# Kernel optimization log

Measured on AMD Instinct MI355X. Metric: run time of the kernel, lower is better.

Reference implementation:

```python
import jax, jax.numpy as jnp
import numpy as np

B, S, E, WIN = 8, 2048, 512, 11  # batch, seq_len, emb_dim, window_size (odd)
PAD_VAL = 0.0  # padding_idx used as constant pad value in F.pad


def setup_inputs() -> dict:
    key = jax.random.key(0)
    k1, k2, k3 = jax.random.split(key, 3)
    x = jax.random.normal(k1, (B, S, E), dtype=jnp.float32)
    lim = 1.0 / np.sqrt(E * WIN)  # torch Linear default init bound
    # One independent Linear per timestep (deepcopy clones): stacked weights/bias
    W = jax.random.uniform(k2, (S, WIN, WIN * E), minval=-lim, maxval=lim, dtype=jnp.float32)
    b = jax.random.uniform(k3, (S, WIN), minval=-lim, maxval=lim, dtype=jnp.float32)
    return {"x": x, "W": W, "b": b}


def reference(x, W, b):
    ww = WIN // 2
    # pad sequence dim on both sides with padding_idx
    padded = jnp.pad(x, ((0, 0), (ww, ww), (0, 0)), constant_values=PAD_VAL)  # [B, S+2ww, E]
    # gather all sliding windows at once: windows[b,t,j,:] = padded[b, t+j, :]
    idx = jnp.arange(S)[:, None] + jnp.arange(WIN)[None, :]
    windows = padded[:, idx, :]
    flat = windows.reshape(B, S, WIN * E)                     # flattened window per position
    gates = jax.nn.sigmoid(jnp.einsum('bsf,swf->bsw', flat, W) + b)
    # gate * embeddings, sum over window, tanh
    score = jnp.einsum('bsw,bswe->bse', gates, windows)       # [B, S, E]
    return jnp.tanh(score)
```

## Files before the change

### kernel.cpp

```cpp
#include <hip/hip_runtime.h>
#include <math.h>

#define B_    8
#define S_    2048
#define E_    512
#define WIN_  11
#define WW    5
#define F4C   1408
#define E4C   128
#define NBLKA (S_ * WIN_)
#define CPX_A (NBLKA / 8)
#define PSTR  (B_ * WIN_)

template <int CTRL, int RMASK>
__device__ __forceinline__ float dpp_add(float v) {
    int sh = __builtin_amdgcn_update_dpp(0, __float_as_int(v),
                                         CTRL, RMASK, 0xF, true);
    return v + __int_as_float(sh);
}
__device__ __forceinline__ float wave_sum63(float v) {
    v = dpp_add<0x111, 0xF>(v);
    v = dpp_add<0x112, 0xF>(v);
    v = dpp_add<0x114, 0xF>(v);
    v = dpp_add<0x118, 0xF>(v);
    v = dpp_add<0x142, 0xA>(v);
    v = dpp_add<0x143, 0xC>(v);
    return v;
}

__global__ __launch_bounds__(256)
void win_gate_partial(const float* __restrict__ x,
                      const float* __restrict__ W,
                      float* __restrict__ P)
{
    const int bid = blockIdx.x;
    const int sw  = (bid & 7) * CPX_A + (bid >> 3);
    const int s   = sw / WIN_;
    const int wp  = sw - s * WIN_;

    const int tid  = threadIdx.x;
    const int wid  = tid >> 6;
    const int lane = tid & 63;

    float* __restrict__ Pblk = P + (size_t)sw * PSTR;

    const int row = s - WW + wp;
    if (row < 0 || row >= S_) {
        if (tid < PSTR) Pblk[tid] = 0.f;
        return;
    }

    const float4* __restrict__ X4 = reinterpret_cast<const float4*>(x);
    const float4* __restrict__ W4 = reinterpret_cast<const float4*>(W)
        + (size_t)s * (WIN_ * F4C) + (size_t)wp * E4C;

    __shared__ float4 Wlds[WIN_ * E4C];

    #pragma unroll
    for (int j = 0; j < 6; ++j) {
        const int m = j * 256 + tid;
        if (j < 5 || wid < 2) {
            const int w  = m >> 7;
            const int e4 = m & 127;
            const float4* src = W4 + (size_t)w * F4C + e4;
            __builtin_amdgcn_global_load_lds(
                (const __attribute__((address_space(1))) void*)src,
                (__attribute__((address_space(3))) void*)&Wlds[m],
                16, 0, 0);
        }
    }
    __syncthreads();

    const int w0   = wid * 3;
    const int wcnt = (wid == 3) ? 2 : 3;

    float4 wv[3][2];
    #pragma unroll
    for (int j = 0; j < 3; ++j)
        if (j < wcnt) {
            wv[j][0] = Wlds[(w0 + j) * E4C + lane];
            wv[j][1] = Wlds[(w0 + j) * E4C + lane + 64];
        }

    float acc[B_][3];
    #pragma unroll
    for (int b = 0; b < B_; ++b)
        #pragma unroll
        for (int j = 0; j < 3; ++j) acc[b][j] = 0.f;

    #pragma unroll
    for (int half = 0; half < 2; ++half) {
        float4 xv[4][2];
        #pragma unroll
        for (int bb = 0; bb < 4; ++bb) {
            const int b = half * 4 + bb;
            xv[bb][0] = X4[((size_t)b * S_ + row) * E4C + lane];
            xv[bb][1] = X4[((size_t)b * S_ + row) * E4C + lane + 64];
        }
        #pragma unroll
        for (int bb = 0; bb < 4; ++bb) {
            const int b = half * 4 + bb;
            #pragma unroll
            for (int j = 0; j < 3; ++j) {
                if (j < wcnt) {
                    float a = acc[b][j];
                    a = fmaf(xv[bb][0].x, wv[j][0].x, a);
                    a = fmaf(xv[bb][0].y, wv[j][0].y, a);
                    a = fmaf(xv[bb][0].z, wv[j][0].z, a);
                    a = fmaf(xv[bb][0].w, wv[j][0].w, a);
                    a = fmaf(xv[bb][1].x, wv[j][1].x, a);
                    a = fmaf(xv[bb][1].y, wv[j][1].y, a);
                    a = fmaf(xv[bb][1].z, wv[j][1].z, a);
                    a = fmaf(xv[bb][1].w, wv[j][1].w, a);
                    acc[b][j] = a;
                }
            }
        }
    }

    #pragma unroll
    for (int b = 0; b < B_; ++b)
        #pragma unroll
        for (int j = 0; j < 3; ++j)
            if (j < wcnt) acc[b][j] = wave_sum63(acc[b][j]);

    if (lane == 63) {
        #pragma unroll
        for (int b = 0; b < B_; ++b)
            #pragma unroll
            for (int j = 0; j < 3; ++j)
                if (j < wcnt) Pblk[b * WIN_ + w0 + j] = acc[b][j];
    }
}

__device__ __forceinline__ float tanh_fast(float v) {
    const float e = __expf(v + v);
    return 1.f - 2.f / (e + 1.f);
}

__global__ __launch_bounds__(256)
void win_score(const float* __restrict__ x,
               const float* __restrict__ bias,
               const float* __restrict__ P,
               float* __restrict__ out)
{
    const int bid = blockIdx.x;
    const int s   = (bid & 7) * (S_ / 8) + (bid >> 3);
    const int tid = threadIdx.x;

    __shared__ float Pl[WIN_ * PSTR];
    __shared__ float gates[PSTR];

    const float4* Ps = reinterpret_cast<const float4*>(P + (size_t)s * (WIN_ * PSTR));
    if (tid < (WIN_ * PSTR) / 4)
        reinterpret_cast<float4*>(Pl)[tid] = Ps[tid];
    __syncthreads();

    if (tid < PSTR) {
        const int w = tid % WIN_;
        float v = bias[s * WIN_ + w];
        #pragma unroll
        for (int wp = 0; wp < WIN_; ++wp) v += Pl[wp * PSTR + tid];
        gates[tid] = 1.f / (1.f + __expf(-v));
    }
    __syncthreads();

    const float4* __restrict__ X4   = reinterpret_cast<const float4*>(x);
    float4* __restrict__       OUT4 = reinterpret_cast<float4*>(out);

    #pragma unroll
    for (int it = 0; it < 4; ++it) {
        const int i  = tid + (it << 8);
        const int b  = i >> 7;
        const int e4 = i & 127;
        float4 sc = make_float4(0.f, 0.f, 0.f, 0.f);
        #pragma unroll
        for (int w = 0; w < WIN_; ++w) {
            const int r = s - WW + w;
            if (r >= 0 && r < S_) {
                const float g   = gates[b * WIN_ + w];
                const float4 xv = X4[((size_t)b * S_ + r) * E4C + e4];
                sc.x = fmaf(g, xv.x, sc.x);
                sc.y = fmaf(g, xv.y, sc.y);
                sc.z = fmaf(g, xv.z, sc.z);
                sc.w = fmaf(g, xv.w, sc.w);
            }
        }
        float4 o;
        o.x = tanh_fast(sc.x);
        o.y = tanh_fast(sc.y);
        o.z = tanh_fast(sc.z);
        o.w = tanh_fast(sc.w);
        OUT4[((size_t)b * S_ + s) * E4C + e4] = o;
    }
}

extern "C" void kernel_launch(void* const* d_in, const int* in_sizes, int n_in,
                              void* d_out, int out_size, void* d_ws, size_t ws_size,
                              hipStream_t stream)
{
    const float* x    = (const float*)d_in[0];
    const float* W    = (const float*)d_in[1];
    const float* bias = (const float*)d_in[2];
    float* out        = (float*)d_out;
    float* P          = (float*)d_ws;

    win_gate_partial<<<dim3(NBLKA), dim3(256), 0, stream>>>(x, W, P);
    win_score<<<dim3(S_), dim3(256), 0, stream>>>(x, bias, P, out);
}
```

Measured before the change: 158.5 us.

## Fuse gate partial and score kernels into one per-timestep kernel

Merges the two kernels into a single kernel with one block per timestep. That block loops over the 11 window positions, stages the weight slice in LDS each iteration and accumulates the gate logits in registers. This removes the partial-sum workspace round trip and one kernel launch. In exchange, grid parallelism drops from S*WIN blocks to S blocks, and each iteration serializes a weight load, a barrier and the compute with no double buffering, so latency hiding may suffer.

New measurement: 156.0 us. About the same (-1.6%).

```diff
diff --git a/kernel.cpp b/kernel.cpp
--- a/kernel.cpp
+++ b/kernel.cpp
@@ -8,8 +8,6 @@
 #define WW    5
 #define F4C   1408
 #define E4C   128
-#define NBLKA (S_ * WIN_)
-#define CPX_A (NBLKA / 8)
 #define PSTR  (B_ * WIN_)
 
 template <int CTRL, int RMASK>
@@ -28,59 +26,32 @@
     return v;
 }
 
+__device__ __forceinline__ float tanh_fast(float v) {
+    const float e = __expf(v + v);
+    return 1.f - 2.f / (e + 1.f);
+}
+
 __global__ __launch_bounds__(256)
-void win_gate_partial(const float* __restrict__ x,
-                      const float* __restrict__ W,
-                      float* __restrict__ P)
+void win_attn_fused(const float* __restrict__ x,
+                    const float* __restrict__ W,
+                    const float* __restrict__ bias,
+                    float* __restrict__ out)
 {
-    const int bid = blockIdx.x;
-    const int sw  = (bid & 7) * CPX_A + (bid >> 3);
-    const int s   = sw / WIN_;
-    const int wp  = sw - s * WIN_;
-
+    const int bid  = blockIdx.x;
+    const int s    = (bid & 7) * (S_ / 8) + (bid >> 3);
     const int tid  = threadIdx.x;
     const int wid  = tid >> 6;
     const int lane = tid & 63;
 
-    float* __restrict__ Pblk = P + (size_t)sw * PSTR;
+    const float4* __restrict__ X4 = reinterpret_cast<const float4*>(x);
+    const float4* __restrict__ Ws = reinterpret_cast<const float4*>(W)
+                                    + (size_t)s * (WIN_ * F4C);
 
-    const int row = s - WW + wp;
-    if (row < 0 || row >= S_) {
-        if (tid < PSTR) Pblk[tid] = 0.f;
-        return;
-    }
-
-    const float4* __restrict__ X4 = reinterpret_cast<const float4*>(x);
-    const float4* __restrict__ W4 = reinterpret_cast<const float4*>(W)
-        + (size_t)s * (WIN_ * F4C) + (size_t)wp * E4C;
-
-    __shared__ float4 Wlds[WIN_ * E4C];
-
-    #pragma unroll
-    for (int j = 0; j < 6; ++j) {
-        const int m = j * 256 + tid;
-        if (j < 5 || wid < 2) {
-            const int w  = m >> 7;
-            const int e4 = m & 127;
-            const float4* src = W4 + (size_t)w * F4C + e4;
-            __builtin_amdgcn_global_load_lds(
-                (const __attribute__((address_space(1))) void*)src,
-                (__attribute__((address_space(3))) void*)&Wlds[m],
-                16, 0, 0);
-        }
-    }
-    __syncthreads();
+    __shared__ float4 Wbuf[WIN_ * E4C];
+    __shared__ float gates[PSTR];
 
     const int w0   = wid * 3;
     const int wcnt = (wid == 3) ? 2 : 3;
-
-    float4 wv[3][2];
-    #pragma unroll
-    for (int j = 0; j < 3; ++j)
-        if (j < wcnt) {
-            wv[j][0] = Wlds[(w0 + j) * E4C + lane];
-            wv[j][1] = Wlds[(w0 + j) * E4C + lane + 64];
-        }
 
     float acc[B_][3];
     #pragma unroll
@@ -88,34 +59,64 @@
         #pragma unroll
         for (int j = 0; j < 3; ++j) acc[b][j] = 0.f;
 
-    #pragma unroll
-    for (int half = 0; half < 2; ++half) {
-        float4 xv[4][2];
+    #pragma unroll 1
+    for (int wp = 0; wp < WIN_; ++wp) {
         #pragma unroll
-        for (int bb = 0; bb < 4; ++bb) {
-            const int b = half * 4 + bb;
-            xv[bb][0] = X4[((size_t)b * S_ + row) * E4C + lane];
-            xv[bb][1] = X4[((size_t)b * S_ + row) * E4C + lane + 64];
+        for (int j = 0; j < 6; ++j) {
+            const int m = j * 256 + tid;
+            if (j < 5 || wid < 2) {
+                const int w  = m >> 7;
+                const int e4 = m & 127;
+                const float4* src = Ws + (size_t)w * F4C + wp * E4C + e4;
+                __builtin_amdgcn_global_load_lds(
+                    (const __attribute__((address_space(1))) void*)src,
+                    (__attribute__((address_space(3))) void*)&Wbuf[m],
+                    16, 0, 0);
+            }
         }
-        #pragma unroll
-        for (int bb = 0; bb < 4; ++bb) {
-            const int b = half * 4 + bb;
+        __syncthreads();
+
+        const int row = s - WW + wp;
+        if (row >= 0 && row < S_) {
+            float4 wv[3][2];
             #pragma unroll
-            for (int j = 0; j < 3; ++j) {
+            for (int j = 0; j < 3; ++j)
                 if (j < wcnt) {
-                    float a = acc[b][j];
-                    a = fmaf(xv[bb][0].x, wv[j][0].x, a);
-                    a = fmaf(xv[bb][0].y, wv[j][0].y, a);
-                    a = fmaf(xv[bb][0].z, wv[j][0].z, a);
-                    a = fmaf(xv[bb][0].w, wv[j][0].w, a);
-                    a = fmaf(xv[bb][1].x, wv[j][1].x, a);
-                    a = fmaf(xv[bb][1].y, wv[j][1].y, a);
-                    a = fmaf(xv[bb][1].z, wv[j][1].z, a);
-                    a = fmaf(xv[bb][1].w, wv[j][1].w, a);
-                    acc[b][j] = a;
+                    wv[j][0] = Wbuf[(w0 + j) * E4C + lane];
+                    wv[j][1] = Wbuf[(w0 + j) * E4C + lane + 64];
+                }
+
+            #pragma unroll
+            for (int half = 0; half < 2; ++half) {
+                float4 xv[4][2];
+                #pragma unroll
+                for (int bb = 0; bb < 4; ++bb) {
+                    const int b = half * 4 + bb;
+                    xv[bb][0] = X4[((size_t)b * S_ + row) * E4C + lane];
+                    xv[bb][1] = X4[((size_t)b * S_ + row) * E4C + lane + 64];
+                }
+                #pragma unroll
+                for (int bb = 0; bb < 4; ++bb) {
+                    const int b = half * 4 + bb;
+                    #pragma unroll
+                    for (int j = 0; j < 3; ++j) {
+                        if (j < wcnt) {
+                            float a = acc[b][j];
+                            a = fmaf(xv[bb][0].x, wv[j][0].x, a);
+                            a = fmaf(xv[bb][0].y, wv[j][0].y, a);
+                            a = fmaf(xv[bb][0].z, wv[j][0].z, a);
+                            a = fmaf(xv[bb][0].w, wv[j][0].w, a);
+                            a = fmaf(xv[bb][1].x, wv[j][1].x, a);
+                            a = fmaf(xv[bb][1].y, wv[j][1].y, a);
+                            a = fmaf(xv[bb][1].z, wv[j][1].z, a);
+                            a = fmaf(xv[bb][1].w, wv[j][1].w, a);
+                            acc[b][j] = a;
+                        }
+                    }
                 }
             }
         }
+        __syncthreads();
     }
 
     #pragma unroll
@@ -129,45 +130,18 @@
         for (int b = 0; b < B_; ++b)
             #pragma unroll
             for (int j = 0; j < 3; ++j)
-                if (j < wcnt) Pblk[b * WIN_ + w0 + j] = acc[b][j];
+                if (j < wcnt) gates[b * WIN_ + w0 + j] = acc[b][j];
     }
-}
-
-__device__ __forceinline__ float tanh_fast(float v) {
-    const float e = __expf(v + v);
-    return 1.f - 2.f / (e + 1.f);
-}
-
-__global__ __launch_bounds__(256)
-void win_score(const float* __restrict__ x,
-               const float* __restrict__ bias,
-               const float* __restrict__ P,
-               float* __restrict__ out)
-{
-    const int bid = blockIdx.x;
-    const int s   = (bid & 7) * (S_ / 8) + (bid >> 3);
-    const int tid = threadIdx.x;
-
-    __shared__ float Pl[WIN_ * PSTR];
-    __shared__ float gates[PSTR];
-
-    const float4* Ps = reinterpret_cast<const float4*>(P + (size_t)s * (WIN_ * PSTR));
-    if (tid < (WIN_ * PSTR) / 4)
-        reinterpret_cast<float4*>(Pl)[tid] = Ps[tid];
     __syncthreads();
 
     if (tid < PSTR) {
         const int w = tid % WIN_;
-        float v = bias[s * WIN_ + w];
-        #pragma unroll
-        for (int wp = 0; wp < WIN_; ++wp) v += Pl[wp * PSTR + tid];
+        const float v = gates[tid] + bias[s * WIN_ + w];
         gates[tid] = 1.f / (1.f + __expf(-v));
     }
     __syncthreads();
 
-    const float4* __restrict__ X4   = reinterpret_cast<const float4*>(x);
-    float4* __restrict__       OUT4 = reinterpret_cast<float4*>(out);
-
+    float4* __restrict__ OUT4 = reinterpret_cast<float4*>(out);
     #pragma unroll
     for (int it = 0; it < 4; ++it) {
         const int i  = tid + (it << 8);
@@ -203,8 +177,6 @@
     const float* W    = (const float*)d_in[1];
     const float* bias = (const float*)d_in[2];
     float* out        = (float*)d_out;
-    float* P          = (float*)d_ws;
 
-    win_gate_partial<<<dim3(NBLKA), dim3(256), 0, stream>>>(x, W, P);
-    win_score<<<dim3(S_), dim3(256), 0, stream>>>(x, bias, P, out);
+    win_attn_fused<<<dim3(S_), dim3(256), 0, stream>>>(x, W, bias, out);
 }
```
